# Kernel optimization log

Measured on AMD Instinct MI355X. Metric: run time of the kernel, lower is better.

Reference implementation:

```python
import jax, jax.numpy as jnp
import numpy as np

NUM_LABELS = 80
GROUPS = 512
OUT_PER_GROUP = 4  # 2048 / 512
K = 14  # kernel == spatial size -> 1x1 output


def setup_inputs() -> dict:
    key = jax.random.key(0)
    ks = jax.random.split(key, 8)
    B = 256
    x = jax.random.normal(ks[0], (B, NUM_LABELS, K, K), dtype=jnp.float32)
    # conv1: 1x1, num_labels -> 512 (store as [out,in])
    w1 = jax.random.normal(ks[1], (512, NUM_LABELS), dtype=jnp.float32) * 0.05
    b1 = jax.random.normal(ks[2], (512,), dtype=jnp.float32) * 0.01
    # conv2: 1x1, 512 -> 512
    w2 = jax.random.normal(ks[3], (512, 512), dtype=jnp.float32) * 0.05
    b2 = jax.random.normal(ks[4], (512,), dtype=jnp.float32) * 0.01
    # conv3 (grouped): per group, 1 in-ch -> 4 out-ch, 14x14 kernel, no bias
    w3 = jax.random.normal(ks[5], (GROUPS, OUT_PER_GROUP, K, K), dtype=jnp.float32) * 0.02
    # fc: 2048 -> num_labels (torch Linear layout [out,in])
    fc_w = jax.random.normal(ks[6], (NUM_LABELS, GROUPS * OUT_PER_GROUP), dtype=jnp.float32) * 0.02
    fc_b = jax.random.normal(ks[7], (NUM_LABELS,), dtype=jnp.float32) * 0.01
    return {"x": x, "w1": w1, "b1": b1, "w2": w2, "b2": b2,
            "w3": w3, "fc_w": fc_w, "fc_b": fc_b}


def reference(x, w1, b1, w2, b2, w3, fc_w, fc_b):
    # conv1: 1x1 conv == channel GEMM. x: [B,C,H,W]
    h = jnp.einsum('bchw,oc->bohw', x, w1) + b1[None, :, None, None]
    # conv2: 1x1 conv, 512 -> 512
    h = jnp.einsum('bchw,oc->bohw', h, w2) + b2[None, :, None, None]
    # conv3: 512 independent group convs (1 in-ch each, full 14x14 kernel,
    # no padding) -> output spatial 1x1. Fused into a single contraction.
    # h: [B, G, H, W], w3: [G, O, H, W] -> [B, G, O]
    g = jnp.einsum('bghw,gohw->bgo', h, w3)
    g = jax.nn.relu(g)
    # torch.cat over groups then flatten == reshape [B, G*O]
    flat = g.reshape(g.shape[0], GROUPS * OUT_PER_GROUP)
    return flat @ fc_w.T + fc_b
```

## Files before the change

kernel.cpp:

```cpp
#include <hip/hip_runtime.h>
#include <hip/hip_bf16.h>

#define CIN 80
#define NSP 196
#define HWP 208
#define KP  96
#define XST 104

#define NBA 1024
#define NBC 512
#define NBD 64

typedef __attribute__((ext_vector_type(8))) short  short8;
typedef __attribute__((ext_vector_type(4))) float  floatx4;
typedef __attribute__((ext_vector_type(4))) unsigned short ushort4v;

static __device__ __forceinline__ unsigned short f2b(float f) {
    __hip_bfloat16 h = __float2bfloat16(f);
    return *(unsigned short*)&h;
}
static __device__ __forceinline__ float b2f(unsigned short u) {
    unsigned int x = ((unsigned int)u) << 16;
    float f; __builtin_memcpy(&f, &x, 4); return f;
}

__global__ __launch_bounds__(384) void kPre(
    const float* __restrict__ w1, const float* __restrict__ b1,
    const float* __restrict__ w2, const float* __restrict__ w3,
    const float* __restrict__ fc_w,
    float* __restrict__ Wcf8, unsigned short* __restrict__ w3tb,
    unsigned short* __restrict__ fcl)
{
    const int blk = blockIdx.x, t = threadIdx.x;

    if (blk < NBA) {
        const int o4 = blk >> 3, kc = blk & 7, m0 = kc * 64;
        if (t < 324) {
            const int lc = t % 81, oi = t / 81;
            const int o = o4 * 4 + oi;
            const float* __restrict__ w2p = w2 + (size_t)o * 512 + m0;
            float part = 0.f;
            if (lc < CIN) {
                const float* __restrict__ w1p = w1 + (size_t)m0 * CIN + lc;
                #pragma unroll 8
                for (int i = 0; i < 64; ++i)
                    part = fmaf(w2p[i], w1p[(size_t)i * CIN], part);
            } else {
                #pragma unroll 8
                for (int i = 0; i < 64; ++i)
                    part = fmaf(w2p[i], b1[m0 + i], part);
            }
            Wcf8[((size_t)kc * 512 + o) * KP + lc] = part;
        }
    } else if (blk < NBA + NBC) {
        const int g = blk - NBA;
        if (t < HWP) {
            ushort4v v;
            #pragma unroll
            for (int o = 0; o < 4; ++o)
                v[o] = f2b((t < NSP) ? w3[(size_t)g * 4 * NSP + o * NSP + t] : 0.f);
            *(ushort4v*)(w3tb + ((size_t)g * HWP + t) * 4) = v;
        }
    } else {
        const int base = (blk - NBA - NBC) * 2560;
        for (int i = t; i < 2560; i += 384) {
            const int idx = base + i;
            fcl[idx] = f2b(fc_w[idx]);
        }
    }
}

__global__ __launch_bounds__(1024) void kRed(
    const float* __restrict__ Wcf8, const float* __restrict__ b2,
    unsigned short* __restrict__ Wcbf)
{
    const int idx = blockIdx.x * 1024 + threadIdx.x;
    const int o = idx / KP, c = idx - o * KP;
    float s = 0.f;
    if (c <= CIN) {
        #pragma unroll
        for (int j = 0; j < 8; ++j)
            s += Wcf8[((size_t)j * 512 + o) * KP + c];
        if (c == CIN) s += b2[o];
    }
    Wcbf[idx] = f2b(s);
}

__global__ __launch_bounds__(1024) void kM(
    const float* __restrict__ x, const unsigned short* __restrict__ Wcbf,
    const unsigned short* __restrict__ w3tb, const unsigned short* __restrict__ fcl,
    const float* __restrict__ fc_b, float* __restrict__ out)
{
    __shared__ __align__(16) unsigned short xs[HWP * XST];
    __shared__ float gl[2048];
    const int b = blockIdx.x, t = threadIdx.x;

    {
        const floatx4* __restrict__ xb4 = (const floatx4*)(x + (size_t)b * CIN * NSP);
        for (int i4 = t; i4 < CIN * 49; i4 += 1024) {
            const int k = i4 / 49, hw4 = (i4 - k * 49) * 4;
            const floatx4 v = xb4[i4];
            xs[(hw4 + 0) * XST + k] = f2b(v[0]);
            xs[(hw4 + 1) * XST + k] = f2b(v[1]);
            xs[(hw4 + 2) * XST + k] = f2b(v[2]);
            xs[(hw4 + 3) * XST + k] = f2b(v[3]);
        }
        for (int idx = t; idx < NSP * 24; idx += 1024) {
            const int hw = idx / 24, k = 80 + (idx - (idx / 24) * 24);
            xs[hw * XST + k] = (k == CIN) ? (unsigned short)0x3F80 : (unsigned short)0;
        }
        for (int idx = t; idx < 12 * XST; idx += 1024) {
            const int hw = NSP + idx / XST, k = idx - (idx / XST) * XST;
            xs[hw * XST + k] = 0;
        }
    }

    const int w = t >> 6, lane = t & 63;
    const int col = lane & 15, quad = lane >> 4;
    const int gb = w * 32;

    short8 A[2][3];
    #pragma unroll
    for (int mt = 0; mt < 2; ++mt) {
        const unsigned short* __restrict__ ap =
            Wcbf + (size_t)(gb + mt * 16 + col) * KP + quad * 8;
        #pragma unroll
        for (int ks = 0; ks < 3; ++ks) A[mt][ks] = *(const short8*)(ap + ks * 32);
    }

    float p[2][4][4];
    #pragma unroll
    for (int mt = 0; mt < 2; ++mt)
        #pragma unroll
        for (int r = 0; r < 4; ++r)
            #pragma unroll
            for (int o = 0; o < 4; ++o) p[mt][r][o] = 0.f;

    const unsigned short* __restrict__ xrow = xs + col * XST + quad * 8;
    const unsigned short* __restrict__ wb0 =
        w3tb + ((size_t)(gb + quad * 4) * HWP + col) * 4;
    const unsigned short* __restrict__ wb1 =
        w3tb + ((size_t)(gb + 16 + quad * 4) * HWP + col) * 4;

    __syncthreads();

    #pragma unroll 1
    for (int nt = 0; nt < 13; ++nt) {
        ushort4v wv0[4], wv1[4];
        #pragma unroll
        for (int r = 0; r < 4; ++r) {
            wv0[r] = *(const ushort4v*)(wb0 + ((size_t)r * HWP + nt * 16) * 4);
            wv1[r] = *(const ushort4v*)(wb1 + ((size_t)r * HWP + nt * 16) * 4);
        }
        const unsigned short* __restrict__ xp = xrow + nt * 16 * XST;
        const short8 x0 = *(const short8*)(xp);
        const short8 x1 = *(const short8*)(xp + 32);
        const short8 x2 = *(const short8*)(xp + 64);
        floatx4 a0 = {0.f, 0.f, 0.f, 0.f}, a1 = {0.f, 0.f, 0.f, 0.f};
        a0 = __builtin_amdgcn_mfma_f32_16x16x32_bf16(A[0][0], x0, a0, 0, 0, 0);
        a0 = __builtin_amdgcn_mfma_f32_16x16x32_bf16(A[0][1], x1, a0, 0, 0, 0);
        a0 = __builtin_amdgcn_mfma_f32_16x16x32_bf16(A[0][2], x2, a0, 0, 0, 0);
        a1 = __builtin_amdgcn_mfma_f32_16x16x32_bf16(A[1][0], x0, a1, 0, 0, 0);
        a1 = __builtin_amdgcn_mfma_f32_16x16x32_bf16(A[1][1], x1, a1, 0, 0, 0);
        a1 = __builtin_amdgcn_mfma_f32_16x16x32_bf16(A[1][2], x2, a1, 0, 0, 0);
        #pragma unroll
        for (int r = 0; r < 4; ++r) {
            p[0][r][0] = fmaf(a0[r], b2f(wv0[r][0]), p[0][r][0]);
            p[0][r][1] = fmaf(a0[r], b2f(wv0[r][1]), p[0][r][1]);
            p[0][r][2] = fmaf(a0[r], b2f(wv0[r][2]), p[0][r][2]);
            p[0][r][3] = fmaf(a0[r], b2f(wv0[r][3]), p[0][r][3]);
            p[1][r][0] = fmaf(a1[r], b2f(wv1[r][0]), p[1][r][0]);
            p[1][r][1] = fmaf(a1[r], b2f(wv1[r][1]), p[1][r][1]);
            p[1][r][2] = fmaf(a1[r], b2f(wv1[r][2]), p[1][r][2]);
            p[1][r][3] = fmaf(a1[r], b2f(wv1[r][3]), p[1][r][3]);
        }
    }

    #pragma unroll
    for (int mt = 0; mt < 2; ++mt)
        #pragma unroll
        for (int r = 0; r < 4; ++r) {
            float q0 = p[mt][r][0], q1 = p[mt][r][1], q2 = p[mt][r][2], q3 = p[mt][r][3];
            #pragma unroll
            for (int s = 8; s >= 1; s >>= 1) {
                q0 += __shfl_down(q0, s, 16);
                q1 += __shfl_down(q1, s, 16);
                q2 += __shfl_down(q2, s, 16);
                q3 += __shfl_down(q3, s, 16);
            }
            if (col == 0) {
                const int glocal = gb + mt * 16 + quad * 4 + r;
                floatx4 ov = {fmaxf(q0, 0.f), fmaxf(q1, 0.f), fmaxf(q2, 0.f), fmaxf(q3, 0.f)};
                *(floatx4*)(gl + glocal * 4) = ov;
            }
        }
    __syncthreads();

    #pragma unroll 1
    for (int rr = 0; rr < 5; ++rr) {
        const int l = w * 5 + rr;
        const unsigned int* __restrict__ fr =
            (const unsigned int*)(fcl + (size_t)l * 2048) + lane;
        const float* __restrict__ gp = gl + lane * 2;
        float s = 0.f;
        #pragma unroll
        for (int j = 0; j < 16; ++j) {
            const unsigned int u = fr[j * 64];
            float lo, hi;
            { unsigned int a = u << 16;          __builtin_memcpy(&lo, &a, 4); }
            { unsigned int a = u & 0xFFFF0000u;  __builtin_memcpy(&hi, &a, 4); }
            s = fmaf(gp[j * 128    ], lo, s);
            s = fmaf(gp[j * 128 + 1], hi, s);
        }
        #pragma unroll
        for (int sft = 32; sft >= 1; sft >>= 1) s += __shfl_down(s, sft, 64);
        if (lane == 0) out[b * CIN + l] = s + fc_b[l];
    }
}

extern "C" void kernel_launch(void* const* d_in, const int* in_sizes, int n_in,
                              void* d_out, int out_size, void* d_ws, size_t ws_size,
                              hipStream_t stream) {
    const float* x    = (const float*)d_in[0];
    const float* w1   = (const float*)d_in[1];
    const float* b1   = (const float*)d_in[2];
    const float* w2   = (const float*)d_in[3];
    const float* b2   = (const float*)d_in[4];
    const float* w3   = (const float*)d_in[5];
    const float* fc_w = (const float*)d_in[6];
    const float* fc_b = (const float*)d_in[7];
    float* out = (float*)d_out;

    const int B = in_sizes[0] / (CIN * NSP);

    char* ws = (char*)d_ws;
    float* Wcf8 = (float*)ws;
    size_t off = (size_t)8 * 512 * KP * 4;
    unsigned short* Wcbf = (unsigned short*)(ws + off); off += 512 * KP * 2;
    unsigned short* w3tb = (unsigned short*)(ws + off); off += (size_t)512 * HWP * 4 * 2;
    unsigned short* fcl  = (unsigned short*)(ws + off);

    kPre<<<NBA + NBC + NBD, 384, 0, stream>>>(w1, b1, w2, w3, fc_w, Wcf8, w3tb, fcl);
    kRed<<<48, 1024, 0, stream>>>(Wcf8, b2, Wcbf);
    kM<<<B, 1024, 0, stream>>>(x, Wcbf, w3tb, fcl, fc_b, out);
}
```

Baseline: 113.5 us.

## Split main kernel across two group-halves per batch with atomic FC accumulation

The main kernel grid becomes (B,2), and each block handles 256 of the 512 groups, so a wave computes one 16-row MFMA tile instead of two. The FC partial sums from the two halves are combined with atomicAdd into an output that the preprocessing kernel pre-fills with fc_b. This doubles block count for better CU occupancy and shortens each block's serial work. In exchange, every half-block re-stages the full x tile into LDS, and float atomics make the result order non-deterministic.

```diff
diff --git a/kernel.cpp b/kernel.cpp
--- a/kernel.cpp
+++ b/kernel.cpp
@@ -10,6 +10,7 @@
 #define NBA 1024
 #define NBC 512
 #define NBD 64
+#define NBE 16
 
 typedef __attribute__((ext_vector_type(8))) short  short8;
 typedef __attribute__((ext_vector_type(4))) float  floatx4;
@@ -27,9 +28,9 @@
 __global__ __launch_bounds__(384) void kPre(
     const float* __restrict__ w1, const float* __restrict__ b1,
     const float* __restrict__ w2, const float* __restrict__ w3,
-    const float* __restrict__ fc_w,
+    const float* __restrict__ fc_w, const float* __restrict__ fc_b,
     float* __restrict__ Wcf8, unsigned short* __restrict__ w3tb,
-    unsigned short* __restrict__ fcl)
+    unsigned short* __restrict__ fcl, float* __restrict__ out)
 {
     const int blk = blockIdx.x, t = threadIdx.x;
 
@@ -61,11 +62,17 @@
                 v[o] = f2b((t < NSP) ? w3[(size_t)g * 4 * NSP + o * NSP + t] : 0.f);
             *(ushort4v*)(w3tb + ((size_t)g * HWP + t) * 4) = v;
         }
-    } else {
+    } else if (blk < NBA + NBC + NBD) {
         const int base = (blk - NBA - NBC) * 2560;
         for (int i = t; i < 2560; i += 384) {
             const int idx = base + i;
             fcl[idx] = f2b(fc_w[idx]);
+        }
+    } else {
+        const int base = (blk - NBA - NBC - NBD) * 1280;
+        for (int i = t; i < 1280; i += 384) {
+            const int idx = base + i;
+            out[idx] = fc_b[idx - (idx / CIN) * CIN];
         }
     }
 }
@@ -89,11 +96,11 @@
 __global__ __launch_bounds__(1024) void kM(
     const float* __restrict__ x, const unsigned short* __restrict__ Wcbf,
     const unsigned short* __restrict__ w3tb, const unsigned short* __restrict__ fcl,
-    const float* __restrict__ fc_b, float* __restrict__ out)
+    float* __restrict__ out)
 {
     __shared__ __align__(16) unsigned short xs[HWP * XST];
-    __shared__ float gl[2048];
-    const int b = blockIdx.x, t = threadIdx.x;
+    __shared__ float gl[1024];
+    const int b = blockIdx.x, h = blockIdx.y, t = threadIdx.x;
 
     {
         const floatx4* __restrict__ xb4 = (const floatx4*)(x + (size_t)b * CIN * NSP);
@@ -117,94 +124,78 @@
 
     const int w = t >> 6, lane = t & 63;
     const int col = lane & 15, quad = lane >> 4;
-    const int gb = w * 32;
-
-    short8 A[2][3];
+    const int g = h * 256 + w * 16;
+
+    short8 A[3];
+    {
+        const unsigned short* __restrict__ ap =
+            Wcbf + (size_t)(g + col) * KP + quad * 8;
+        #pragma unroll
+        for (int ks = 0; ks < 3; ++ks) A[ks] = *(const short8*)(ap + ks * 32);
+    }
+
+    float p[4][4];
     #pragma unroll
-    for (int mt = 0; mt < 2; ++mt) {
-        const unsigned short* __restrict__ ap =
-            Wcbf + (size_t)(gb + mt * 16 + col) * KP + quad * 8;
-        #pragma unroll
-        for (int ks = 0; ks < 3; ++ks) A[mt][ks] = *(const short8*)(ap + ks * 32);
-    }
-
-    float p[2][4][4];
-    #pragma unroll
-    for (int mt = 0; mt < 2; ++mt)
-        #pragma unroll
-        for (int r = 0; r < 4; ++r)
-            #pragma unroll
-            for (int o = 0; o < 4; ++o) p[mt][r][o] = 0.f;
+    for (int r = 0; r < 4; ++r)
+        #pragma unroll
+        for (int o = 0; o < 4; ++o) p[r][o] = 0.f;
 
     const unsigned short* __restrict__ xrow = xs + col * XST + quad * 8;
-    const unsigned short* __restrict__ wb0 =
-        w3tb + ((size_t)(gb + quad * 4) * HWP + col) * 4;
-    const unsigned short* __restrict__ wb1 =
-        w3tb + ((size_t)(gb + 16 + quad * 4) * HWP + col) * 4;
+    const unsigned short* __restrict__ wb =
+        w3tb + ((size_t)(g + quad * 4) * HWP + col) * 4;
 
     __syncthreads();
 
     #pragma unroll 1
     for (int nt = 0; nt < 13; ++nt) {
-        ushort4v wv0[4], wv1[4];
-        #pragma unroll
-        for (int r = 0; r < 4; ++r) {
-            wv0[r] = *(const ushort4v*)(wb0 + ((size_t)r * HWP + nt * 16) * 4);
-            wv1[r] = *(const ushort4v*)(wb1 + ((size_t)r * HWP + nt * 16) * 4);
-        }
+        ushort4v wv[4];
+        #pragma unroll
+        for (int r = 0; r < 4; ++r)
+            wv[r] = *(const ushort4v*)(wb + ((size_t)r * HWP + nt * 16) * 4);
         const unsigned short* __restrict__ xp = xrow + nt * 16 * XST;
         const short8 x0 = *(const short8*)(xp);
         const short8 x1 = *(const short8*)(xp + 32);
         const short8 x2 = *(const short8*)(xp + 64);
-        floatx4 a0 = {0.f, 0.f, 0.f, 0.f}, a1 = {0.f, 0.f, 0.f, 0.f};
-        a0 = __builtin_amdgcn_mfma_f32_16x16x32_bf16(A[0][0], x0, a0, 0, 0, 0);
-        a0 = __builtin_amdgcn_mfma_f32_16x16x32_bf16(A[0][1], x1, a0, 0, 0, 0);
-        a0 = __builtin_amdgcn_mfma_f32_16x16x32_bf16(A[0][2], x2, a0, 0, 0, 0);
-        a1 = __builtin_amdgcn_mfma_f32_16x16x32_bf16(A[1][0], x0, a1, 0, 0, 0);
-        a1 = __builtin_amdgcn_mfma_f32_16x16x32_bf16(A[1][1], x1, a1, 0, 0, 0);
-        a1 = __builtin_amdgcn_mfma_f32_16x16x32_bf16(A[1][2], x2, a1, 0, 0, 0);
+        floatx4 a0 = {0.f, 0.f, 0.f, 0.f};
+        a0 = __builtin_amdgcn_mfma_f32_16x16x32_bf16(A[0], x0, a0, 0, 0, 0);
+        a0 = __builtin_amdgcn_mfma_f32_16x16x32_bf16(A[1], x1, a0, 0, 0, 0);
+        a0 = __builtin_amdgcn_mfma_f32_16x16x32_bf16(A[2], x2, a0, 0, 0, 0);
         #pragma unroll
         for (int r = 0; r < 4; ++r) {
-            p[0][r][0] = fmaf(a0[r], b2f(wv0[r][0]), p[0][r][0]);
-            p[0][r][1] = fmaf(a0[r], b2f(wv0[r][1]), p[0][r][1]);
-            p[0][r][2] = fmaf(a0[r], b2f(wv0[r][2]), p[0][r][2]);
-            p[0][r][3] = fmaf(a0[r], b2f(wv0[r][3]), p[0][r][3]);
-            p[1][r][0] = fmaf(a1[r], b2f(wv1[r][0]), p[1][r][0]);
-            p[1][r][1] = fmaf(a1[r], b2f(wv1[r][1]), p[1][r][1]);
-            p[1][r][2] = fmaf(a1[r], b2f(wv1[r][2]), p[1][r][2]);
-            p[1][r][3] = fmaf(a1[r], b2f(wv1[r][3]), p[1][r][3]);
+            p[r][0] = fmaf(a0[r], b2f(wv[r][0]), p[r][0]);
+            p[r][1] = fmaf(a0[r], b2f(wv[r][1]), p[r][1]);
+            p[r][2] = fmaf(a0[r], b2f(wv[r][2]), p[r][2]);
+            p[r][3] = fmaf(a0[r], b2f(wv[r][3]), p[r][3]);
         }
     }
 
     #pragma unroll
-    for (int mt = 0; mt < 2; ++mt)
-        #pragma unroll
-        for (int r = 0; r < 4; ++r) {
-            float q0 = p[mt][r][0], q1 = p[mt][r][1], q2 = p[mt][r][2], q3 = p[mt][r][3];
-            #pragma unroll
-            for (int s = 8; s >= 1; s >>= 1) {
-                q0 += __shfl_down(q0, s, 16);
-                q1 += __shfl_down(q1, s, 16);
-                q2 += __shfl_down(q2, s, 16);
-                q3 += __shfl_down(q3, s, 16);
-            }
-            if (col == 0) {
-                const int glocal = gb + mt * 16 + quad * 4 + r;
-                floatx4 ov = {fmaxf(q0, 0.f), fmaxf(q1, 0.f), fmaxf(q2, 0.f), fmaxf(q3, 0.f)};
-                *(floatx4*)(gl + glocal * 4) = ov;
-            }
-        }
+    for (int r = 0; r < 4; ++r) {
+        float q0 = p[r][0], q1 = p[r][1], q2 = p[r][2], q3 = p[r][3];
+        #pragma unroll
+        for (int s = 8; s >= 1; s >>= 1) {
+            q0 += __shfl_down(q0, s, 16);
+            q1 += __shfl_down(q1, s, 16);
+            q2 += __shfl_down(q2, s, 16);
+            q3 += __shfl_down(q3, s, 16);
+        }
+        if (col == 0) {
+            const int glocal = w * 16 + quad * 4 + r;
+            floatx4 ov = {fmaxf(q0, 0.f), fmaxf(q1, 0.f), fmaxf(q2, 0.f), fmaxf(q3, 0.f)};
+            *(floatx4*)(gl + glocal * 4) = ov;
+        }
+    }
     __syncthreads();
 
     #pragma unroll 1
     for (int rr = 0; rr < 5; ++rr) {
         const int l = w * 5 + rr;
         const unsigned int* __restrict__ fr =
-            (const unsigned int*)(fcl + (size_t)l * 2048) + lane;
+            (const unsigned int*)(fcl + (size_t)l * 2048 + h * 1024) + lane;
         const float* __restrict__ gp = gl + lane * 2;
         float s = 0.f;
         #pragma unroll
-        for (int j = 0; j < 16; ++j) {
+        for (int j = 0; j < 8; ++j) {
             const unsigned int u = fr[j * 64];
             float lo, hi;
             { unsigned int a = u << 16;          __builtin_memcpy(&lo, &a, 4); }
@@ -214,7 +205,7 @@
         }
         #pragma unroll
         for (int sft = 32; sft >= 1; sft >>= 1) s += __shfl_down(s, sft, 64);
-        if (lane == 0) out[b * CIN + l] = s + fc_b[l];
+        if (lane == 0) atomicAdd(out + b * CIN + l, s);
     }
 }
 
@@ -240,7 +231,8 @@
     unsigned short* w3tb = (unsigned short*)(ws + off); off += (size_t)512 * HWP * 4 * 2;
     unsigned short* fcl  = (unsigned short*)(ws + off);
 
-    kPre<<<NBA + NBC + NBD, 384, 0, stream>>>(w1, b1, w2, w3, fc_w, Wcf8, w3tb, fcl);
+    kPre<<<NBA + NBC + NBD + NBE, 384, 0, stream>>>(
+        w1, b1, w2, w3, fc_w, fc_b, Wcf8, w3tb, fcl, out);
     kRed<<<48, 1024, 0, stream>>>(Wcf8, b2, Wcbf);
-    kM<<<B, 1024, 0, stream>>>(x, Wcbf, w3tb, fcl, fc_b, out);
-}
+    kM<<<dim3(B, 2), 1024, 0, stream>>>(x, Wcbf, w3tb, fcl, out);
+}
```

Result: no change. 115.0 us (+1.4%).
